# Kernel optimization log

Hardware: AMD Instinct MI355X
Metric: run time of the kernel (lower is better)

The kernel has to match this reference:

```python
import jax, jax.numpy as jnp
import numpy as np

B, D = 8192, 1024
HR, HE, HF = 512, 4096, 2048
N_OPS, N_TASKS = 4, 4

def setup_inputs() -> dict:
    key = jax.random.key(0)
    ks = jax.random.split(key, 20)
    s = 0.02
    return {
        "x":        jax.random.normal(ks[0], (B, D), jnp.float32),
        # router
        "W_r1":   s*jax.random.normal(ks[1], (D, HR), jnp.float32),
        "b_r1":     jnp.zeros((HR,), jnp.float32),
        "W_dom":  s*jax.random.normal(ks[2], (HR, 2), jnp.float32),
        "b_dom":    jnp.zeros((2,), jnp.float32),
        "W_mop":  s*jax.random.normal(ks[3], (HR, N_OPS), jnp.float32),
        "W_lt":   s*jax.random.normal(ks[4], (HR, N_TASKS), jnp.float32),
        # math expert (operation hint = additive embedding)
        "op_emb": s*jax.random.normal(ks[5], (N_OPS, D), jnp.float32),
        "W_m1":   s*jax.random.normal(ks[6], (D, HE), jnp.float32),
        "b_m1":     jnp.zeros((HE,), jnp.float32),
        "W_m2":   s*jax.random.normal(ks[7], (HE, D), jnp.float32),
        "b_m2":     jnp.zeros((D,), jnp.float32),
        # language expert (task hint = additive embedding)
        "task_emb": s*jax.random.normal(ks[8], (N_TASKS, D), jnp.float32),
        "W_l1":   s*jax.random.normal(ks[9], (D, HE), jnp.float32),
        "b_l1":     jnp.zeros((HE,), jnp.float32),
        "W_l2":   s*jax.random.normal(ks[10], (HE, D), jnp.float32),
        "b_l2":     jnp.zeros((D,), jnp.float32),
        # fusion
        "W_f1":   s*jax.random.normal(ks[11], (D, HF), jnp.float32),
        "b_f1":     jnp.zeros((HF,), jnp.float32),
        "W_f2":   s*jax.random.normal(ks[12], (HF, D), jnp.float32),
        "b_f2":     jnp.zeros((D,), jnp.float32),
    }

def reference(x, W_r1, b_r1, W_dom, b_dom, W_mop, W_lt,
              op_emb, W_m1, b_m1, W_m2, b_m2,
              task_emb, W_l1, b_l1, W_l2, b_l2,
              W_f1, b_f1, W_f2, b_f2):
    # --- router ---
    h = jax.nn.relu(x @ W_r1 + b_r1)                      # [B, HR]
    dom_logits = h @ W_dom + b_dom                        # [B, 2]
    expert_weights = jax.nn.softmax(dom_logits, axis=-1)  # [B, 2]
    primary = jnp.argmax(dom_logits, axis=-1)             # [B]
    math_op = jnp.argmax(h @ W_mop, axis=-1)              # [B]
    lang_task = jnp.argmax(h @ W_lt, axis=-1)             # [B]
    # --- experts (vectorized equivalent of per-sample dispatch) ---
    math_in = x + op_emb[math_op]                         # [B, D]
    math_out = jax.nn.relu(math_in @ W_m1 + b_m1) @ W_m2 + b_m2
    lang_in = x + task_emb[lang_task]                     # [B, D]
    lang_out = jax.nn.relu(lang_in @ W_l1 + b_l1) @ W_l2 + b_l2
    selected = jnp.where((primary == 0)[:, None], math_out, lang_out)  # [B, D]
    # --- fusion: scale by routing weight of the chosen expert + MLP residual ---
    w = jnp.take_along_axis(expert_weights, primary[:, None], axis=1)  # [B, 1]
    fused = w * selected
    final = fused + jax.nn.relu(fused @ W_f1 + b_f1) @ W_f2 + b_f2     # [B, D]
    return final
```

## Files before the change

### kernel.cpp

```cpp
#include <hip/hip_runtime.h>
#include <hip/hip_bf16.h>
#include <stdint.h>

#define NB 8192
#define DD 1024
#define HRD 512
#define HED 4096
#define HFD 2048

typedef __attribute__((ext_vector_type(8))) short bf16x8;
typedef __attribute__((ext_vector_type(4))) float f32x4;
typedef unsigned short u16;

__device__ __forceinline__ u16 f2b(float f) {
    union { float f; uint32_t i; } c; c.f = f;
    uint32_t r = c.i + 0x7FFF + ((c.i >> 16) & 1);
    return (u16)(r >> 16);
}
__device__ __forceinline__ float b2f(u16 u) {
    union { uint32_t i; float f; } c; c.i = ((uint32_t)u) << 16; return c.f;
}
__device__ __forceinline__ void glds16(const char* g, char* l) {
    __builtin_amdgcn_global_load_lds((const __attribute__((address_space(1))) void*)g,
                                     (__attribute__((address_space(3))) void*)l, 16, 0, 0);
}

__global__ void k_init(int* cnt) { if (threadIdx.x < 2) cnt[threadIdx.x] = 0; }

__global__ __launch_bounds__(256) void k_split(const float4* __restrict__ x4,
                                               ushort4* __restrict__ hi4,
                                               ushort4* __restrict__ lo4) {
    int i = blockIdx.x * 256 + threadIdx.x;
    float4 v = x4[i];
    ushort4 h, l;
    h.x = f2b(v.x); l.x = f2b(v.x - b2f(h.x));
    h.y = f2b(v.y); l.y = f2b(v.y - b2f(h.y));
    h.z = f2b(v.z); l.z = f2b(v.z - b2f(h.z));
    h.w = f2b(v.w); l.w = f2b(v.w - b2f(h.w));
    hi4[i] = h; lo4[i] = l;
}

__global__ __launch_bounds__(256) void k_transpose(const float* __restrict__ in,
                                                   u16* __restrict__ out, int R, int C) {
    __shared__ float s[64][65];
    int tx = threadIdx.x & 63, ty = threadIdx.x >> 6;
    int c0 = blockIdx.x * 64, r0 = blockIdx.y * 64;
#pragma unroll
    for (int j = 0; j < 16; j++) { int r = ty + j * 4; s[r][tx] = in[(size_t)(r0 + r) * C + c0 + tx]; }
    __syncthreads();
#pragma unroll
    for (int j = 0; j < 16; j++) { int c = ty + j * 4; out[(size_t)(c0 + c) * R + r0 + tx] = f2b(s[tx][c]); }
}

__global__ __launch_bounds__(256) void k_transpose_split(const float* __restrict__ in,
                                                         u16* __restrict__ ohi, u16* __restrict__ olo,
                                                         int R, int C) {
    __shared__ float s[64][65];
    int tx = threadIdx.x & 63, ty = threadIdx.x >> 6;
    int c0 = blockIdx.x * 64, r0 = blockIdx.y * 64;
#pragma unroll
    for (int j = 0; j < 16; j++) { int r = ty + j * 4; s[r][tx] = in[(size_t)(r0 + r) * C + c0 + tx]; }
    __syncthreads();
#pragma unroll
    for (int j = 0; j < 16; j++) {
        int c = ty + j * 4;
        float v = s[tx][c];
        u16 h = f2b(v);
        ohi[(size_t)(c0 + c) * R + r0 + tx] = h;
        olo[(size_t)(c0 + c) * R + r0 + tx] = f2b(v - b2f(h));
    }
}

__global__ __launch_bounds__(256) void k_router(const u16* __restrict__ Ah, const u16* __restrict__ Al,
                                                const u16* __restrict__ Bh, const u16* __restrict__ Bl,
                                                const float* __restrict__ bias, float* __restrict__ H) {
    __shared__ u16 sAh[64 * 64], sAl[64 * 64], sBh[128 * 64], sBl[128 * 64];
    int tid = threadIdx.x, lane = tid & 63, wave = tid >> 6;
    int bm = blockIdx.x, bn = blockIdx.y;
    f32x4 acc[2][4];
#pragma unroll
    for (int i = 0; i < 2; i++)
#pragma unroll
        for (int j = 0; j < 4; j++) acc[i][j] = (f32x4)0.f;
    int wm = (wave & 1) * 32, wn = (wave >> 1) * 64;
    const long ks = DD * 2;
    const char* ahB = (const char*)Ah + (size_t)bm * 64 * ks;
    const char* alB = (const char*)Al + (size_t)bm * 64 * ks;
    const char* bhB = (const char*)Bh + (size_t)bn * 128 * ks;
    const char* blB = (const char*)Bl + (size_t)bn * 128 * ks;
    for (int k0 = 0; k0 < DD; k0 += 64) {
#pragma unroll
        for (int is = 0; is < 2; is++) {
            int c = wave * 2 + is;
            long go = (long)(c * 8 + (lane >> 3)) * ks + k0 * 2 + (lane & 7) * 16;
            glds16(ahB + go, (char*)sAh + c * 1024);
            glds16(alB + go, (char*)sAl + c * 1024);
        }
#pragma unroll
        for (int is = 0; is < 4; is++) {
            int c = wave * 4 + is;
            long go = (long)(c * 8 + (lane >> 3)) * ks + k0 * 2 + (lane & 7) * 16;
            glds16(bhB + go, (char*)sBh + c * 1024);
            glds16(blB + go, (char*)sBl + c * 1024);
        }
        __syncthreads();
#pragma unroll
        for (int kk = 0; kk < 2; kk++) {
            int kofs = kk * 64 + (lane >> 4) * 16;
            bf16x8 vbh[4], vbl[4];
#pragma unroll
            for (int ni = 0; ni < 4; ni++) {
                int rB = (wn + ni * 16 + (lane & 15)) * 128 + kofs;
                vbh[ni] = *(const bf16x8*)((const char*)sBh + rB);
                vbl[ni] = *(const bf16x8*)((const char*)sBl + rB);
            }
#pragma unroll
            for (int mi = 0; mi < 2; mi++) {
                int rA = (wm + mi * 16 + (lane & 15)) * 128 + kofs;
                bf16x8 vah = *(const bf16x8*)((const char*)sAh + rA);
                bf16x8 val = *(const bf16x8*)((const char*)sAl + rA);
#pragma unroll
                for (int ni = 0; ni < 4; ni++) {
                    acc[mi][ni] = __builtin_amdgcn_mfma_f32_16x16x32_bf16(vah, vbh[ni], acc[mi][ni], 0, 0, 0);
                    acc[mi][ni] = __builtin_amdgcn_mfma_f32_16x16x32_bf16(vah, vbl[ni], acc[mi][ni], 0, 0, 0);
                    acc[mi][ni] = __builtin_amdgcn_mfma_f32_16x16x32_bf16(val, vbh[ni], acc[mi][ni], 0, 0, 0);
                }
            }
        }
        __syncthreads();
    }
    int quad = lane >> 4, cl = lane & 15;
#pragma unroll
    for (int mi = 0; mi < 2; mi++)
#pragma unroll
        for (int r = 0; r < 4; r++) {
            int row = bm * 64 + wm + mi * 16 + quad * 4 + r;
#pragma unroll
            for (int ni = 0; ni < 4; ni++) {
                int col = bn * 128 + wn + ni * 16 + cl;
                float v = acc[mi][ni][r] + bias[col];
                H[(size_t)row * HRD + col] = fmaxf(v, 0.f);
            }
        }
}

__global__ __launch_bounds__(256) void k_heads(const float* __restrict__ H,
                                               const float* __restrict__ Wd, const float* __restrict__ bd,
                                               const float* __restrict__ Wm, const float* __restrict__ Wl,
                                               int* __restrict__ cnt, int* __restrict__ perm,
                                               float* __restrict__ wsc, int* __restrict__ eic) {
    int lane = threadIdx.x & 63, wave = threadIdx.x >> 6;
    int r = blockIdx.x * 4 + wave;
    const float4* h4 = (const float4*)(H + (size_t)r * HRD);
    float4 v0 = h4[lane * 2], v1 = h4[lane * 2 + 1];
    float hv[8] = {v0.x, v0.y, v0.z, v0.w, v1.x, v1.y, v1.z, v1.w};
    float a[10];
#pragma unroll
    for (int t = 0; t < 10; t++) a[t] = 0.f;
    int kbase = lane * 8;
#pragma unroll
    for (int j = 0; j < 8; j++) {
        int k = kbase + j;
        float h_ = hv[j];
        float2 wd = ((const float2*)Wd)[k];
        a[0] += h_ * wd.x; a[1] += h_ * wd.y;
        float4 wm = ((const float4*)Wm)[k];
        a[2] += h_ * wm.x; a[3] += h_ * wm.y; a[4] += h_ * wm.z; a[5] += h_ * wm.w;
        float4 wl = ((const float4*)Wl)[k];
        a[6] += h_ * wl.x; a[7] += h_ * wl.y; a[8] += h_ * wl.z; a[9] += h_ * wl.w;
    }
#pragma unroll
    for (int t = 0; t < 10; t++)
#pragma unroll
        for (int off = 32; off > 0; off >>= 1) a[t] += __shfl_down(a[t], off);
    if (lane == 0) {
        float d0 = a[0] + bd[0], d1 = a[1] + bd[1];
        int primary = (d1 > d0) ? 1 : 0;
        float w = 1.f / (1.f + expf(-fabsf(d0 - d1)));
        int mi = 0; float mv = a[2];
        if (a[3] > mv) { mv = a[3]; mi = 1; }
        if (a[4] > mv) { mv = a[4]; mi = 2; }
        if (a[5] > mv) { mv = a[5]; mi = 3; }
        int li = 0; float lv = a[6];
        if (a[7] > lv) { lv = a[7]; li = 1; }
        if (a[8] > lv) { lv = a[8]; li = 2; }
        if (a[9] > lv) { lv = a[9]; li = 3; }
        int pos;
        if (primary == 0) pos = atomicAdd(&cnt[0], 1);
        else              pos = NB - 1 - atomicAdd(&cnt[1], 1);
        perm[pos] = r; wsc[pos] = w; eic[pos] = (primary == 0) ? mi : li;
    }
}

__global__ __launch_bounds__(256) void k_gather(const float* __restrict__ x,
                                                const float* __restrict__ op_emb,
                                                const float* __restrict__ task_emb,
                                                const int* __restrict__ perm, const int* __restrict__ eic,
                                                const int* __restrict__ cnt, u16* __restrict__ xin) {
    int lane = threadIdx.x & 63, wave = threadIdx.x >> 6;
    int i = blockIdx.x * 4 + wave;
    int n0 = cnt[0];
    int r = perm[i];
    const float* emb = ((i >= n0) ? task_emb : op_emb) + (size_t)eic[i] * DD;
    const float4* x4 = (const float4*)(x + (size_t)r * DD);
    const float4* e4 = (const float4*)emb;
    ushort4* o4 = (ushort4*)(xin + (size_t)i * DD);
#pragma unroll
    for (int j = 0; j < 4; j++) {
        int idx = lane + j * 64;
        float4 xv = x4[idx], ev = e4[idx];
        ushort4 o;
        o.x = f2b(xv.x + ev.x); o.y = f2b(xv.y + ev.y);
        o.z = f2b(xv.z + ev.z); o.w = f2b(xv.w + ev.w);
        o4[idx] = o;
    }
}

template <int EPI, bool DUAL>
__global__ __launch_bounds__(256) void k_gemm64(const u16* __restrict__ A,
                                                const u16* __restrict__ Btm, const u16* __restrict__ Btl,
                                                const float* __restrict__ biasm, const float* __restrict__ biasl,
                                                void* __restrict__ Out, int K, int N,
                                                const int* __restrict__ cnt, const float* __restrict__ wsel,
                                                const int* __restrict__ perm, const u16* __restrict__ resid) {
    __shared__ u16 sA[64 * 64];
    __shared__ u16 sB[256 * 64];
    int tid = threadIdx.x, lane = tid & 63, wave = tid >> 6;
    int t = blockIdx.x, bn = blockIdx.y;
    int tile = t, storeLo, storeHi;
    const u16* Bt = Btm; const float* bias = biasm;
    if constexpr (DUAL) {
        int n0 = cnt[0];
        int tb = n0 >> 6;
        bool isMath = (t <= tb) && (t < NB / 64);
        tile = isMath ? t : t - 1;
        int lo = tile * 64, hi = lo + 64;
        if (isMath) { storeLo = lo; storeHi = n0 < hi ? n0 : hi; }
        else        { storeLo = n0 > lo ? n0 : lo; storeHi = hi; }
        if (storeLo >= storeHi) return;
        if (!isMath) { Bt = Btl; bias = biasl; }
    } else {
        storeLo = t * 64; storeHi = storeLo + 64;
    }
    f32x4 acc[4][4];
#pragma unroll
    for (int i = 0; i < 4; i++)
#pragma unroll
        for (int j = 0; j < 4; j++) acc[i][j] = (f32x4)0.f;
    int wn = wave * 64;
    const long ks = (long)K * 2;
    const char* aBase = (const char*)A + (size_t)tile * 64 * ks;
    const char* bBase = (const char*)Bt + (size_t)bn * 256 * ks;
    for (int k0 = 0; k0 < K; k0 += 64) {
#pragma unroll
        for (int is = 0; is < 2; is++) {
            int c = wave * 2 + is;
            long go = (long)(c * 8 + (lane >> 3)) * ks + k0 * 2 + (lane & 7) * 16;
            glds16(aBase + go, (char*)sA + c * 1024);
        }
#pragma unroll
        for (int is = 0; is < 8; is++) {
            int c = wave * 8 + is;
            long go = (long)(c * 8 + (lane >> 3)) * ks + k0 * 2 + (lane & 7) * 16;
            glds16(bBase + go, (char*)sB + c * 1024);
        }
        __syncthreads();
#pragma unroll
        for (int kk = 0; kk < 2; kk++) {
            int kofs = kk * 64 + (lane >> 4) * 16;
            bf16x8 vb[4];
#pragma unroll
            for (int ni = 0; ni < 4; ni++)
                vb[ni] = *(const bf16x8*)((const char*)sB + (wn + ni * 16 + (lane & 15)) * 128 + kofs);
#pragma unroll
            for (int mi = 0; mi < 4; mi++) {
                bf16x8 va = *(const bf16x8*)((const char*)sA + (mi * 16 + (lane & 15)) * 128 + kofs);
#pragma unroll
                for (int ni = 0; ni < 4; ni++)
                    acc[mi][ni] = __builtin_amdgcn_mfma_f32_16x16x32_bf16(va, vb[ni], acc[mi][ni], 0, 0, 0);
            }
        }
        __syncthreads();
    }
    int quad = lane >> 4, cl = lane & 15;
#pragma unroll
    for (int mi = 0; mi < 4; mi++)
#pragma unroll
        for (int r = 0; r < 4; r++) {
            int grow = tile * 64 + mi * 16 + quad * 4 + r;
            if (grow < storeLo || grow >= storeHi) continue;
            float wrow = 0.f;
            if constexpr (EPI == 1) wrow = wsel[grow];
#pragma unroll
            for (int ni = 0; ni < 4; ni++) {
                int col = bn * 256 + wn + ni * 16 + cl;
                float v = acc[mi][ni][r] + bias[col];
                if constexpr (EPI == 0) {
                    ((u16*)Out)[(size_t)grow * N + col] = f2b(fmaxf(v, 0.f));
                } else if constexpr (EPI == 1) {
                    ((u16*)Out)[(size_t)grow * N + col] = f2b(v * wrow);
                } else {
                    v += b2f(resid[(size_t)grow * N + col]);
                    ((float*)Out)[(size_t)perm[grow] * N + col] = v;
                }
            }
        }
}

extern "C" void kernel_launch(void* const* d_in, const int* in_sizes, int n_in,
                              void* d_out, int out_size, void* d_ws, size_t ws_size,
                              hipStream_t stream) {
    const float* x      = (const float*)d_in[0];
    const float* W_r1   = (const float*)d_in[1];
    const float* b_r1   = (const float*)d_in[2];
    const float* W_dom  = (const float*)d_in[3];
    const float* b_dom  = (const float*)d_in[4];
    const float* W_mop  = (const float*)d_in[5];
    const float* W_lt   = (const float*)d_in[6];
    const float* op_emb = (const float*)d_in[7];
    const float* W_m1   = (const float*)d_in[8];
    const float* b_m1   = (const float*)d_in[9];
    const float* W_m2   = (const float*)d_in[10];
    const float* b_m2   = (const float*)d_in[11];
    const float* task_emb = (const float*)d_in[12];
    const float* W_l1   = (const float*)d_in[13];
    const float* b_l1   = (const float*)d_in[14];
    const float* W_l2   = (const float*)d_in[15];
    const float* b_l2   = (const float*)d_in[16];
    const float* W_f1   = (const float*)d_in[17];
    const float* b_f1   = (const float*)d_in[18];
    const float* W_f2   = (const float*)d_in[19];
    const float* b_f2   = (const float*)d_in[20];

    char* wsp = (char*)d_ws;
    size_t off = 0;
    auto take = [&](size_t bytes) -> char* {
        char* p = wsp + off;
        off += (bytes + 255) & ~(size_t)255;
        return p;
    };
    u16* Wr_hi = (u16*)take((size_t)HRD * DD * 2);
    u16* Wr_lo = (u16*)take((size_t)HRD * DD * 2);
    u16* Wm1t  = (u16*)take((size_t)HED * DD * 2);
    u16* Wl1t  = (u16*)take((size_t)HED * DD * 2);
    u16* Wm2t  = (u16*)take((size_t)DD * HED * 2);
    u16* Wl2t  = (u16*)take((size_t)DD * HED * 2);
    u16* Wf1t  = (u16*)take((size_t)HFD * DD * 2);
    u16* Wf2t  = (u16*)take((size_t)DD * HFD * 2);
    u16* x_hi  = (u16*)take((size_t)NB * DD * 2);
    u16* x_lo  = (u16*)take((size_t)NB * DD * 2);
    float* Hbuf = (float*)take((size_t)NB * HRD * 4);
    u16* hid   = (u16*)take((size_t)NB * HED * 2);
    int* cnt   = (int*)take(256);
    int* perm  = (int*)take(NB * 4);
    int* eic   = (int*)take(NB * 4);
    float* wsc = (float*)take(NB * 4);
    u16* xin   = x_hi;
    u16* fused = x_lo;
    u16* hid2  = Wm1t;

    k_init<<<1, 64, 0, stream>>>(cnt);
    k_split<<<(NB * DD / 4) / 256, 256, 0, stream>>>((const float4*)x, (ushort4*)x_hi, (ushort4*)x_lo);
    k_transpose_split<<<dim3(HRD / 64, DD / 64), 256, 0, stream>>>(W_r1, Wr_hi, Wr_lo, DD, HRD);
    k_transpose<<<dim3(HED / 64, DD / 64), 256, 0, stream>>>(W_m1, Wm1t, DD, HED);
    k_transpose<<<dim3(HED / 64, DD / 64), 256, 0, stream>>>(W_l1, Wl1t, DD, HED);
    k_transpose<<<dim3(DD / 64, HED / 64), 256, 0, stream>>>(W_m2, Wm2t, HED, DD);
    k_transpose<<<dim3(DD / 64, HED / 64), 256, 0, stream>>>(W_l2, Wl2t, HED, DD);
    k_transpose<<<dim3(HFD / 64, DD / 64), 256, 0, stream>>>(W_f1, Wf1t, DD, HFD);
    k_transpose<<<dim3(DD / 64, HFD / 64), 256, 0, stream>>>(W_f2, Wf2t, HFD, DD);

    k_router<<<dim3(NB / 64, HRD / 128), 256, 0, stream>>>(x_hi, x_lo, Wr_hi, Wr_lo, b_r1, Hbuf);
    k_heads<<<NB / 4, 256, 0, stream>>>(Hbuf, W_dom, b_dom, W_mop, W_lt, cnt, perm, wsc, eic);
    k_gather<<<NB / 4, 256, 0, stream>>>(x, op_emb, task_emb, perm, eic, cnt, xin);

    k_gemm64<0, true><<<dim3(NB / 64 + 1, HED / 256), 256, 0, stream>>>(
        xin, Wm1t, Wl1t, b_m1, b_l1, hid, DD, HED, cnt, nullptr, nullptr, nullptr);
    k_gemm64<1, true><<<dim3(NB / 64 + 1, DD / 256), 256, 0, stream>>>(
        hid, Wm2t, Wl2t, b_m2, b_l2, fused, HED, DD, cnt, wsc, nullptr, nullptr);
    k_gemm64<0, false><<<dim3(NB / 64, HFD / 256), 256, 0, stream>>>(
        fused, Wf1t, nullptr, b_f1, nullptr, hid2, DD, HFD, nullptr, nullptr, nullptr, nullptr);
    k_gemm64<2, false><<<dim3(NB / 64, DD / 256), 256, 0, stream>>>(
        hid2, Wf2t, nullptr, b_f2, nullptr, d_out, HFD, DD, nullptr, nullptr, perm, fused);
}
```

Measured before the change: 771.4 us.

## Double-buffer GEMMs with 128x128 tiles and fold router split-bf16 into concatenated-K GEMM

Replaces the 64x256 single-buffered GEMM with a 128x128 tile kernel that double-buffers A and B in LDS, so global-to-LDS loads for the next K step overlap MFMA work on the current one. The dedicated 3-MFMA router kernel is removed. Its hi/lo bf16 split is instead expressed as a single GEMM over a concatenated K of 3072 ([xh,xh,xl] x [Wh,Wl,Wh]), reusing the generic kernel with a new fp32 ReLU epilogue. The grid is now ordered with N blocks along x. The trade-off is twice the LDS per block, which may lower occupancy, plus a tripled-width A buffer for the router.

```diff
diff --git a/kernel.cpp b/kernel.cpp
--- a/kernel.cpp
+++ b/kernel.cpp
@@ -7,6 +7,7 @@
 #define HRD 512
 #define HED 4096
 #define HFD 2048
+#define KR3 3072
 
 typedef __attribute__((ext_vector_type(8))) short bf16x8;
 typedef __attribute__((ext_vector_type(4))) float f32x4;
@@ -27,17 +28,18 @@
 
 __global__ void k_init(int* cnt) { if (threadIdx.x < 2) cnt[threadIdx.x] = 0; }
 
-__global__ __launch_bounds__(256) void k_split(const float4* __restrict__ x4,
-                                               ushort4* __restrict__ hi4,
-                                               ushort4* __restrict__ lo4) {
-    int i = blockIdx.x * 256 + threadIdx.x;
-    float4 v = x4[i];
+__global__ __launch_bounds__(256) void k_split3(const float4* __restrict__ x4,
+                                                ushort4* __restrict__ a3) {
+    int i4 = blockIdx.x * 256 + threadIdx.x;
+    int row = i4 >> 8, c4 = i4 & 255;
+    float4 v = x4[i4];
     ushort4 h, l;
     h.x = f2b(v.x); l.x = f2b(v.x - b2f(h.x));
     h.y = f2b(v.y); l.y = f2b(v.y - b2f(h.y));
     h.z = f2b(v.z); l.z = f2b(v.z - b2f(h.z));
     h.w = f2b(v.w); l.w = f2b(v.w - b2f(h.w));
-    hi4[i] = h; lo4[i] = l;
+    ushort4* ob = a3 + (size_t)row * 768;
+    ob[c4] = h; ob[c4 + 256] = h; ob[c4 + 512] = l;
 }
 
 __global__ __launch_bounds__(256) void k_transpose(const float* __restrict__ in,
@@ -52,9 +54,8 @@
     for (int j = 0; j < 16; j++) { int c = ty + j * 4; out[(size_t)(c0 + c) * R + r0 + tx] = f2b(s[tx][c]); }
 }
 
-__global__ __launch_bounds__(256) void k_transpose_split(const float* __restrict__ in,
-                                                         u16* __restrict__ ohi, u16* __restrict__ olo,
-                                                         int R, int C) {
+__global__ __launch_bounds__(256) void k_transpose3(const float* __restrict__ in,
+                                                    u16* __restrict__ out, int R, int C) {
     __shared__ float s[64][65];
     int tx = threadIdx.x & 63, ty = threadIdx.x >> 6;
     int c0 = blockIdx.x * 64, r0 = blockIdx.y * 64;
@@ -66,82 +67,10 @@
         int c = ty + j * 4;
         float v = s[tx][c];
         u16 h = f2b(v);
-        ohi[(size_t)(c0 + c) * R + r0 + tx] = h;
-        olo[(size_t)(c0 + c) * R + r0 + tx] = f2b(v - b2f(h));
-    }
-}
-
-__global__ __launch_bounds__(256) void k_router(const u16* __restrict__ Ah, const u16* __restrict__ Al,
-                                                const u16* __restrict__ Bh, const u16* __restrict__ Bl,
-                                                const float* __restrict__ bias, float* __restrict__ H) {
-    __shared__ u16 sAh[64 * 64], sAl[64 * 64], sBh[128 * 64], sBl[128 * 64];
-    int tid = threadIdx.x, lane = tid & 63, wave = tid >> 6;
-    int bm = blockIdx.x, bn = blockIdx.y;
-    f32x4 acc[2][4];
-#pragma unroll
-    for (int i = 0; i < 2; i++)
-#pragma unroll
-        for (int j = 0; j < 4; j++) acc[i][j] = (f32x4)0.f;
-    int wm = (wave & 1) * 32, wn = (wave >> 1) * 64;
-    const long ks = DD * 2;
-    const char* ahB = (const char*)Ah + (size_t)bm * 64 * ks;
-    const char* alB = (const char*)Al + (size_t)bm * 64 * ks;
-    const char* bhB = (const char*)Bh + (size_t)bn * 128 * ks;
-    const char* blB = (const char*)Bl + (size_t)bn * 128 * ks;
-    for (int k0 = 0; k0 < DD; k0 += 64) {
-#pragma unroll
-        for (int is = 0; is < 2; is++) {
-            int c = wave * 2 + is;
-            long go = (long)(c * 8 + (lane >> 3)) * ks + k0 * 2 + (lane & 7) * 16;
-            glds16(ahB + go, (char*)sAh + c * 1024);
-            glds16(alB + go, (char*)sAl + c * 1024);
-        }
-#pragma unroll
-        for (int is = 0; is < 4; is++) {
-            int c = wave * 4 + is;
-            long go = (long)(c * 8 + (lane >> 3)) * ks + k0 * 2 + (lane & 7) * 16;
-            glds16(bhB + go, (char*)sBh + c * 1024);
-            glds16(blB + go, (char*)sBl + c * 1024);
-        }
-        __syncthreads();
-#pragma unroll
-        for (int kk = 0; kk < 2; kk++) {
-            int kofs = kk * 64 + (lane >> 4) * 16;
-            bf16x8 vbh[4], vbl[4];
-#pragma unroll
-            for (int ni = 0; ni < 4; ni++) {
-                int rB = (wn + ni * 16 + (lane & 15)) * 128 + kofs;
-                vbh[ni] = *(const bf16x8*)((const char*)sBh + rB);
-                vbl[ni] = *(const bf16x8*)((const char*)sBl + rB);
-            }
-#pragma unroll
-            for (int mi = 0; mi < 2; mi++) {
-                int rA = (wm + mi * 16 + (lane & 15)) * 128 + kofs;
-                bf16x8 vah = *(const bf16x8*)((const char*)sAh + rA);
-                bf16x8 val = *(const bf16x8*)((const char*)sAl + rA);
-#pragma unroll
-                for (int ni = 0; ni < 4; ni++) {
-                    acc[mi][ni] = __builtin_amdgcn_mfma_f32_16x16x32_bf16(vah, vbh[ni], acc[mi][ni], 0, 0, 0);
-                    acc[mi][ni] = __builtin_amdgcn_mfma_f32_16x16x32_bf16(vah, vbl[ni], acc[mi][ni], 0, 0, 0);
-                    acc[mi][ni] = __builtin_amdgcn_mfma_f32_16x16x32_bf16(val, vbh[ni], acc[mi][ni], 0, 0, 0);
-                }
-            }
-        }
-        __syncthreads();
-    }
-    int quad = lane >> 4, cl = lane & 15;
-#pragma unroll
-    for (int mi = 0; mi < 2; mi++)
-#pragma unroll
-        for (int r = 0; r < 4; r++) {
-            int row = bm * 64 + wm + mi * 16 + quad * 4 + r;
-#pragma unroll
-            for (int ni = 0; ni < 4; ni++) {
-                int col = bn * 128 + wn + ni * 16 + cl;
-                float v = acc[mi][ni][r] + bias[col];
-                H[(size_t)row * HRD + col] = fmaxf(v, 0.f);
-            }
-        }
+        u16 l = f2b(v - b2f(h));
+        u16* ob = out + (size_t)(c0 + c) * KR3 + r0 + tx;
+        ob[0] = h; ob[DD] = l; ob[2 * DD] = h;
+    }
 }
 
 __global__ __launch_bounds__(256) void k_heads(const float* __restrict__ H,
@@ -216,92 +145,106 @@
     }
 }
 
+__device__ __forceinline__ void stage_tile(const char* gBase, long rowStrideBytes,
+                                           u16* s, int tid) {
+    int wave = tid >> 6, lane = tid & 63;
+#pragma unroll
+    for (int is = 0; is < 4; ++is) {
+        int c = wave * 4 + is;
+        long go = (long)(c * 8 + (lane >> 3)) * rowStrideBytes + (lane & 7) * 16;
+        glds16(gBase + go, (char*)s + c * 1024);
+    }
+}
+
 template <int EPI, bool DUAL>
-__global__ __launch_bounds__(256) void k_gemm64(const u16* __restrict__ A,
-                                                const u16* __restrict__ Btm, const u16* __restrict__ Btl,
-                                                const float* __restrict__ biasm, const float* __restrict__ biasl,
-                                                void* __restrict__ Out, int K, int N,
-                                                const int* __restrict__ cnt, const float* __restrict__ wsel,
-                                                const int* __restrict__ perm, const u16* __restrict__ resid) {
-    __shared__ u16 sA[64 * 64];
-    __shared__ u16 sB[256 * 64];
+__global__ __launch_bounds__(256) void k_gemm_db(const u16* __restrict__ A,
+                                                 const u16* __restrict__ Btm, const u16* __restrict__ Btl,
+                                                 const float* __restrict__ biasm, const float* __restrict__ biasl,
+                                                 void* __restrict__ Out, int K, int N,
+                                                 const int* __restrict__ cnt, const float* __restrict__ wsel,
+                                                 const int* __restrict__ perm, const u16* __restrict__ resid) {
+    __shared__ u16 sA[2][128 * 64];
+    __shared__ u16 sB[2][128 * 64];
     int tid = threadIdx.x, lane = tid & 63, wave = tid >> 6;
-    int t = blockIdx.x, bn = blockIdx.y;
+    int bn = blockIdx.x, t = blockIdx.y;
     int tile = t, storeLo, storeHi;
     const u16* Bt = Btm; const float* bias = biasm;
     if constexpr (DUAL) {
         int n0 = cnt[0];
-        int tb = n0 >> 6;
-        bool isMath = (t <= tb) && (t < NB / 64);
+        int tb = n0 >> 7;
+        bool isMath = (t <= tb) && (t < NB / 128);
         tile = isMath ? t : t - 1;
-        int lo = tile * 64, hi = lo + 64;
+        int lo = tile * 128, hi = lo + 128;
         if (isMath) { storeLo = lo; storeHi = n0 < hi ? n0 : hi; }
         else        { storeLo = n0 > lo ? n0 : lo; storeHi = hi; }
         if (storeLo >= storeHi) return;
         if (!isMath) { Bt = Btl; bias = biasl; }
     } else {
-        storeLo = t * 64; storeHi = storeLo + 64;
+        storeLo = t * 128; storeHi = storeLo + 128;
     }
     f32x4 acc[4][4];
 #pragma unroll
     for (int i = 0; i < 4; i++)
 #pragma unroll
         for (int j = 0; j < 4; j++) acc[i][j] = (f32x4)0.f;
-    int wn = wave * 64;
+    int wm = (wave & 1) * 64, wn = (wave >> 1) * 64;
     const long ks = (long)K * 2;
-    const char* aBase = (const char*)A + (size_t)tile * 64 * ks;
-    const char* bBase = (const char*)Bt + (size_t)bn * 256 * ks;
-    for (int k0 = 0; k0 < K; k0 += 64) {
-#pragma unroll
-        for (int is = 0; is < 2; is++) {
-            int c = wave * 2 + is;
-            long go = (long)(c * 8 + (lane >> 3)) * ks + k0 * 2 + (lane & 7) * 16;
-            glds16(aBase + go, (char*)sA + c * 1024);
+    const char* aBase = (const char*)A + (size_t)tile * 128 * ks;
+    const char* bBase = (const char*)Bt + (size_t)bn * 128 * ks;
+
+    stage_tile(aBase, ks, sA[0], tid);
+    stage_tile(bBase, ks, sB[0], tid);
+    __syncthreads();
+    int cur = 0;
+    for (int k0 = 64; ; k0 += 64) {
+        bool more = (k0 < K);
+        if (more) {
+            stage_tile(aBase + (long)k0 * 2, ks, sA[cur ^ 1], tid);
+            stage_tile(bBase + (long)k0 * 2, ks, sB[cur ^ 1], tid);
         }
-#pragma unroll
-        for (int is = 0; is < 8; is++) {
-            int c = wave * 8 + is;
-            long go = (long)(c * 8 + (lane >> 3)) * ks + k0 * 2 + (lane & 7) * 16;
-            glds16(bBase + go, (char*)sB + c * 1024);
-        }
-        __syncthreads();
+        const u16* cA = sA[cur];
+        const u16* cB = sB[cur];
 #pragma unroll
         for (int kk = 0; kk < 2; kk++) {
             int kofs = kk * 64 + (lane >> 4) * 16;
             bf16x8 vb[4];
 #pragma unroll
             for (int ni = 0; ni < 4; ni++)
-                vb[ni] = *(const bf16x8*)((const char*)sB + (wn + ni * 16 + (lane & 15)) * 128 + kofs);
+                vb[ni] = *(const bf16x8*)((const char*)cB + (wn + ni * 16 + (lane & 15)) * 128 + kofs);
 #pragma unroll
             for (int mi = 0; mi < 4; mi++) {
-                bf16x8 va = *(const bf16x8*)((const char*)sA + (mi * 16 + (lane & 15)) * 128 + kofs);
+                bf16x8 va = *(const bf16x8*)((const char*)cA + (wm + mi * 16 + (lane & 15)) * 128 + kofs);
 #pragma unroll
                 for (int ni = 0; ni < 4; ni++)
                     acc[mi][ni] = __builtin_amdgcn_mfma_f32_16x16x32_bf16(va, vb[ni], acc[mi][ni], 0, 0, 0);
             }
         }
+        if (!more) break;
         __syncthreads();
+        cur ^= 1;
     }
     int quad = lane >> 4, cl = lane & 15;
 #pragma unroll
     for (int mi = 0; mi < 4; mi++)
 #pragma unroll
         for (int r = 0; r < 4; r++) {
-            int grow = tile * 64 + mi * 16 + quad * 4 + r;
+            int grow = tile * 128 + wm + mi * 16 + quad * 4 + r;
             if (grow < storeLo || grow >= storeHi) continue;
             float wrow = 0.f;
             if constexpr (EPI == 1) wrow = wsel[grow];
 #pragma unroll
             for (int ni = 0; ni < 4; ni++) {
-                int col = bn * 256 + wn + ni * 16 + cl;
+                int col = bn * 128 + wn + ni * 16 + cl;
                 float v = acc[mi][ni][r] + bias[col];
                 if constexpr (EPI == 0) {
                     ((u16*)Out)[(size_t)grow * N + col] = f2b(fmaxf(v, 0.f));
                 } else if constexpr (EPI == 1) {
                     ((u16*)Out)[(size_t)grow * N + col] = f2b(v * wrow);
-                } else {
+                } else if constexpr (EPI == 2) {
                     v += b2f(resid[(size_t)grow * N + col]);
                     ((float*)Out)[(size_t)perm[grow] * N + col] = v;
+                } else {
+                    ((float*)Out)[(size_t)grow * N + col] = fmaxf(v, 0.f);
                 }
             }
         }
@@ -339,29 +282,27 @@
         off += (bytes + 255) & ~(size_t)255;
         return p;
     };
-    u16* Wr_hi = (u16*)take((size_t)HRD * DD * 2);
-    u16* Wr_lo = (u16*)take((size_t)HRD * DD * 2);
+    u16* Brt   = (u16*)take((size_t)HRD * KR3 * 2);
     u16* Wm1t  = (u16*)take((size_t)HED * DD * 2);
     u16* Wl1t  = (u16*)take((size_t)HED * DD * 2);
     u16* Wm2t  = (u16*)take((size_t)DD * HED * 2);
     u16* Wl2t  = (u16*)take((size_t)DD * HED * 2);
     u16* Wf1t  = (u16*)take((size_t)HFD * DD * 2);
     u16* Wf2t  = (u16*)take((size_t)DD * HFD * 2);
-    u16* x_hi  = (u16*)take((size_t)NB * DD * 2);
-    u16* x_lo  = (u16*)take((size_t)NB * DD * 2);
+    u16* hid   = (u16*)take((size_t)NB * HED * 2);
     float* Hbuf = (float*)take((size_t)NB * HRD * 4);
-    u16* hid   = (u16*)take((size_t)NB * HED * 2);
+    u16* xin   = (u16*)take((size_t)NB * DD * 2);
+    u16* fused = (u16*)take((size_t)NB * DD * 2);
     int* cnt   = (int*)take(256);
     int* perm  = (int*)take(NB * 4);
     int* eic   = (int*)take(NB * 4);
     float* wsc = (float*)take(NB * 4);
-    u16* xin   = x_hi;
-    u16* fused = x_lo;
+    u16* Abig  = hid;
     u16* hid2  = Wm1t;
 
     k_init<<<1, 64, 0, stream>>>(cnt);
-    k_split<<<(NB * DD / 4) / 256, 256, 0, stream>>>((const float4*)x, (ushort4*)x_hi, (ushort4*)x_lo);
-    k_transpose_split<<<dim3(HRD / 64, DD / 64), 256, 0, stream>>>(W_r1, Wr_hi, Wr_lo, DD, HRD);
+    k_split3<<<(NB * DD / 4) / 256, 256, 0, stream>>>((const float4*)x, (ushort4*)Abig);
+    k_transpose3<<<dim3(HRD / 64, DD / 64), 256, 0, stream>>>(W_r1, Brt, DD, HRD);
     k_transpose<<<dim3(HED / 64, DD / 64), 256, 0, stream>>>(W_m1, Wm1t, DD, HED);
     k_transpose<<<dim3(HED / 64, DD / 64), 256, 0, stream>>>(W_l1, Wl1t, DD, HED);
     k_transpose<<<dim3(DD / 64, HED / 64), 256, 0, stream>>>(W_m2, Wm2t, HED, DD);
@@ -369,16 +310,17 @@
     k_transpose<<<dim3(HFD / 64, DD / 64), 256, 0, stream>>>(W_f1, Wf1t, DD, HFD);
     k_transpose<<<dim3(DD / 64, HFD / 64), 256, 0, stream>>>(W_f2, Wf2t, HFD, DD);
 
-    k_router<<<dim3(NB / 64, HRD / 128), 256, 0, stream>>>(x_hi, x_lo, Wr_hi, Wr_lo, b_r1, Hbuf);
+    k_gemm_db<3, false><<<dim3(HRD / 128, NB / 128), 256, 0, stream>>>(
+        Abig, Brt, nullptr, b_r1, nullptr, Hbuf, KR3, HRD, nullptr, nullptr, nullptr, nullptr);
     k_heads<<<NB / 4, 256, 0, stream>>>(Hbuf, W_dom, b_dom, W_mop, W_lt, cnt, perm, wsc, eic);
     k_gather<<<NB / 4, 256, 0, stream>>>(x, op_emb, task_emb, perm, eic, cnt, xin);
 
-    k_gemm64<0, true><<<dim3(NB / 64 + 1, HED / 256), 256, 0, stream>>>(
+    k_gemm_db<0, true><<<dim3(HED / 128, NB / 128 + 1), 256, 0, stream>>>(
         xin, Wm1t, Wl1t, b_m1, b_l1, hid, DD, HED, cnt, nullptr, nullptr, nullptr);
-    k_gemm64<1, true><<<dim3(NB / 64 + 1, DD / 256), 256, 0, stream>>>(
+    k_gemm_db<1, true><<<dim3(DD / 128, NB / 128 + 1), 256, 0, stream>>>(
         hid, Wm2t, Wl2t, b_m2, b_l2, fused, HED, DD, cnt, wsc, nullptr, nullptr);
-    k_gemm64<0, false><<<dim3(NB / 64, HFD / 256), 256, 0, stream>>>(
+    k_gemm_db<0, false><<<dim3(HFD / 128, NB / 128), 256, 0, stream>>>(
         fused, Wf1t, nullptr, b_f1, nullptr, hid2, DD, HFD, nullptr, nullptr, nullptr, nullptr);
-    k_gemm64<2, false><<<dim3(NB / 64, DD / 256), 256, 0, stream>>>(
+    k_gemm_db<2, false><<<dim3(DD / 128, NB / 128), 256, 0, stream>>>(
         hid2, Wf2t, nullptr, b_f2, nullptr, d_out, HFD, DD, nullptr, nullptr, perm, fused);
 }
```

Result: slower. 840.4 us (+8.9%).
